# Optimization experiments

Hardware: AMD Instinct MI355X
Metric: run time of the kernel (lower is better)

## Reference

```python
import jax, jax.numpy as jnp
import numpy as np

N_NODES = 50000
N_EDGES = 800000
D = 128


def _gcn_layer(x, src, dst, deg_inv_sqrt, W, b, n_nodes):
    # GCNConv: X' = D^{-1/2} (A + I) D^{-1/2} X W + b   (PyG default, self-loops added)
    h = x @ W  # [N, D]
    norm = deg_inv_sqrt[src] * deg_inv_sqrt[dst]  # [E+N]
    msgs = h[src] * norm[:, None]  # [E+N, D] gather + scale
    out = jax.ops.segment_sum(msgs, dst, num_segments=n_nodes)  # scatter-add
    return out + b


def setup_inputs() -> dict:
    key = jax.random.key(0)
    k1, k2, k3, k4 = jax.random.split(key, 4)
    x = jax.random.normal(k1, (N_NODES, D), dtype=jnp.float32)
    edge_index = jax.random.randint(k2, (2, N_EDGES), 0, N_NODES, dtype=jnp.int64)
    scale = 1.0 / np.sqrt(D)
    W1 = jax.random.normal(k3, (D, D), dtype=jnp.float32) * scale
    b1 = jnp.zeros((D,), dtype=jnp.float32)
    W2 = jax.random.normal(k4, (D, D), dtype=jnp.float32) * scale
    b2 = jnp.zeros((D,), dtype=jnp.float32)
    return {"x": x, "edge_index": edge_index, "W1": W1, "b1": b1, "W2": W2, "b2": b2}


def reference(x, edge_index, W1, b1, W2, b2):
    n_nodes = x.shape[0]
    # add self-loops once (same graph both layers)
    loop = jnp.arange(n_nodes, dtype=edge_index.dtype)
    src = jnp.concatenate([edge_index[0], loop])
    dst = jnp.concatenate([edge_index[1], loop])
    deg = jax.ops.segment_sum(jnp.ones_like(dst, dtype=x.dtype), dst, num_segments=n_nodes)
    deg_inv_sqrt = jnp.where(deg > 0, jax.lax.rsqrt(deg), 0.0)

    h = _gcn_layer(x, src, dst, deg_inv_sqrt, W1, b1, n_nodes)
    h = jax.nn.relu(h)
    h = _gcn_layer(h, src, dst, deg_inv_sqrt, W2, b2, n_nodes)
    h = jax.nn.relu(h)
    return h
```

## Files before the change

### kernel.cpp

```cpp
#include <hip/hip_runtime.h>

#define N_NODES 50000
#define N_EDGES 800000
#define D 128
#define NB 392
#define CHUNK 2048
#define NBKT 391
#define LHM (NBKT * NB)
#define NSB ((LHM + 255) / 256)

typedef unsigned int uint32;
typedef unsigned short ushort;
typedef __attribute__((ext_vector_type(8))) short s8v;
typedef __attribute__((ext_vector_type(4))) float f4v;

__device__ __forceinline__ ushort f2bf(float f) {
    unsigned u = __float_as_uint(f);
    u += 0x7FFFu + ((u >> 16) & 1u);
    return (ushort)(u >> 16);
}
__device__ __forceinline__ float bf_lo(uint32 u) { return __uint_as_float(u << 16); }
__device__ __forceinline__ float bf_hi(uint32 u) { return __uint_as_float(u & 0xFFFF0000u); }

__device__ __forceinline__ int block_incl_scan(int v, int t) {
    int lane = t & 63, wv = t >> 6;
    int incl = v;
    #pragma unroll
    for (int off = 1; off < 64; off <<= 1) {
        int u = __shfl_up(incl, off, 64);
        if (lane >= off) incl += u;
    }
    __shared__ int wsums[4];
    if (lane == 63) wsums[wv] = incl;
    __syncthreads();
    int add = 0;
    if (wv > 0) add += wsums[0];
    if (wv > 1) add += wsums[1];
    if (wv > 2) add += wsums[2];
    return incl + add;
}

__global__ __launch_bounds__(256) void phaseA_kernel(const int* __restrict__ dst,
                                                     int* __restrict__ histM,
                                                     const float* __restrict__ W1,
                                                     const float* __restrict__ W2,
                                                     ushort* __restrict__ W1t,
                                                     ushort* __restrict__ W2t) {
    __shared__ int cnt[NBKT];
    int t = threadIdx.x, blk = blockIdx.x;
    if (blk >= NB) {
        const float* W = (blk - NB) ? W2 : W1;
        ushort* Wt = (blk - NB) ? W2t : W1t;
        #pragma unroll
        for (int it = 0; it < 16; it++) {
            int fid = t + it * 256;
            int k = fid >> 5;
            int n0 = (fid & 31) * 4;
            float4 w = ((const float4*)W)[fid];
            Wt[(n0 + 0) * D + k] = f2bf(w.x);
            Wt[(n0 + 1) * D + k] = f2bf(w.y);
            Wt[(n0 + 2) * D + k] = f2bf(w.z);
            Wt[(n0 + 3) * D + k] = f2bf(w.w);
        }
        return;
    }
    for (int i = t; i < NBKT; i += 256) cnt[i] = 0;
    __syncthreads();
    int e0 = blk * CHUNK;
    for (int i = t; i < CHUNK; i += 256) {
        int e = e0 + i;
        if (e < N_EDGES) atomicAdd(&cnt[dst[e] >> 7], 1);
    }
    __syncthreads();
    for (int i = t; i < NBKT; i += 256)
        histM[i * NB + blk] = cnt[i];
}

__global__ __launch_bounds__(256) void scan1g(const int* __restrict__ in,
                                              int* __restrict__ out,
                                              int* __restrict__ bsum) {
    int t = threadIdx.x, blk = blockIdx.x;
    int i = blk * 256 + t;
    int v = (i < LHM) ? in[i] : 0;
    int incl = block_incl_scan(v, t);
    if (i < LHM) out[i] = incl - v;
    if (t == 255) bsum[blk] = incl;
}

__global__ __launch_bounds__(256) void scan23g(int* __restrict__ out,
                                               const int* __restrict__ bsum) {
    int t = threadIdx.x, blk = blockIdx.x;
    int local = 0;
    for (int i = t; i < blk; i += 256) local += bsum[i];
    int lane = t & 63, wv = t >> 6;
    #pragma unroll
    for (int off = 32; off > 0; off >>= 1) local += __shfl_down(local, off, 64);
    __shared__ int ws[4];
    if (lane == 0) ws[wv] = local;
    __syncthreads();
    int boff = ws[0] + ws[1] + ws[2] + ws[3];
    int i = blk * 256 + t;
    if (i < LHM) out[i] += boff;
}

__global__ __launch_bounds__(256) void phaseC_kernel(const int* __restrict__ src,
                                                     const int* __restrict__ dst,
                                                     const int* __restrict__ base,
                                                     uint32* __restrict__ edgeTmp) {
    __shared__ int cur[NBKT];
    int t = threadIdx.x, blk = blockIdx.x;
    for (int i = t; i < NBKT; i += 256) cur[i] = base[i * NB + blk];
    __syncthreads();
    int e0 = blk * CHUNK;
    for (int i = t; i < CHUNK; i += 256) {
        int e = e0 + i;
        if (e < N_EDGES) {
            uint32 s = (uint32)src[e], d = (uint32)dst[e];
            int p = atomicAdd(&cur[d >> 7], 1);
            edgeTmp[p] = (s << 16) | d;
        }
    }
}

__global__ __launch_bounds__(256) void phaseD_kernel(const uint32* __restrict__ edgeTmp,
                                                     const int* __restrict__ base,
                                                     int* __restrict__ rowstart,
                                                     float* __restrict__ dis,
                                                     ushort* __restrict__ e16) {
    __shared__ int cnt[128];
    __shared__ int cur[128];
    int t = threadIdx.x, b = blockIdx.x;
    int beg = base[b * NB];
    int end = (b == NBKT - 1) ? N_EDGES : base[(b + 1) * NB];
    if (t < 128) cnt[t] = 0;
    __syncthreads();
    for (int p = beg + t; p < end; p += 256)
        atomicAdd(&cnt[edgeTmp[p] & 127], 1);
    __syncthreads();
    int c = (t < 128) ? cnt[t] : 0;
    int incl = block_incl_scan(c, t);
    int excl = incl - c;
    int node = b * 128 + t;
    if (t <= 128 && node <= N_NODES) {
        if (t < 128) rowstart[node] = beg + excl;
    }
    if (t == 128 && node <= N_NODES) rowstart[node] = end;
    if (t < 128 && node < N_NODES) dis[node] = rsqrtf((float)(c + 1));
    if (t < 128) cur[t] = excl;
    __syncthreads();
    for (int p = beg + t; p < end; p += 256) {
        uint32 u = edgeTmp[p];
        int r = atomicAdd(&cur[u & 127], 1);
        e16[beg + r] = (ushort)(u >> 16);
    }
}

template<bool BF16IN>
__global__ __launch_bounds__(256) void gemm_mfma(const void* __restrict__ Xv,
                                                 const ushort* __restrict__ Wt,
                                                 const float* __restrict__ dis,
                                                 ushort* __restrict__ Hb) {
    __shared__ ushort Cs[128 * 136];
    int t = threadIdx.x;
    int wv = t >> 6, lane = t & 63;
    int q = lane >> 4, m = lane & 15;
    int rbase = blockIdx.x * 128 + wv * 32;
    f4v zero = {0.f, 0.f, 0.f, 0.f};
    f4v acc[2][8];
    #pragma unroll
    for (int mt = 0; mt < 2; mt++)
        #pragma unroll
        for (int n = 0; n < 8; n++) acc[mt][n] = zero;

    #pragma unroll
    for (int kt = 0; kt < 4; kt++) {
        int k0 = kt * 32 + q * 8;
        s8v a[2];
        #pragma unroll
        for (int mt = 0; mt < 2; mt++) {
            int row = rbase + mt * 16 + m;
            if (row >= N_NODES) row = N_NODES - 1;
            if (BF16IN) {
                const ushort* xp = (const ushort*)Xv + (size_t)row * D + k0;
                a[mt] = *(const s8v*)xp;
            } else {
                const float* xp = (const float*)Xv + (size_t)row * D + k0;
                float4 u0 = *(const float4*)xp;
                float4 u1 = *(const float4*)(xp + 4);
                s8v av;
                av[0] = (short)f2bf(u0.x); av[1] = (short)f2bf(u0.y);
                av[2] = (short)f2bf(u0.z); av[3] = (short)f2bf(u0.w);
                av[4] = (short)f2bf(u1.x); av[5] = (short)f2bf(u1.y);
                av[6] = (short)f2bf(u1.z); av[7] = (short)f2bf(u1.w);
                a[mt] = av;
            }
        }
        #pragma unroll
        for (int n = 0; n < 8; n++) {
            s8v b = *(const s8v*)(Wt + (size_t)(n * 16 + m) * D + k0);
            acc[0][n] = __builtin_amdgcn_mfma_f32_16x16x32_bf16(a[0], b, acc[0][n], 0, 0, 0);
            acc[1][n] = __builtin_amdgcn_mfma_f32_16x16x32_bf16(a[1], b, acc[1][n], 0, 0, 0);
        }
    }
    float disv[2][4];
    #pragma unroll
    for (int mt = 0; mt < 2; mt++)
        #pragma unroll
        for (int r = 0; r < 4; r++) {
            int row = rbase + mt * 16 + q * 4 + r;
            if (row >= N_NODES) row = N_NODES - 1;
            disv[mt][r] = dis[row];
        }
    #pragma unroll
    for (int mt = 0; mt < 2; mt++)
        #pragma unroll
        for (int n = 0; n < 8; n++)
            #pragma unroll
            for (int r = 0; r < 4; r++) {
                int row = wv * 32 + mt * 16 + q * 4 + r;
                Cs[row * 136 + n * 16 + m] = f2bf(acc[mt][n][r] * disv[mt][r]);
            }
    __syncthreads();
    int gbase = blockIdx.x * 128;
    #pragma unroll
    for (int it = 0; it < 8; it++) {
        int cid = t + it * 256;
        int row = cid >> 4, off = (cid & 15) * 8;
        int grow = gbase + row;
        if (grow < N_NODES) {
            s8v v = *(const s8v*)(Cs + row * 136 + off);
            *(s8v*)(Hb + (size_t)grow * D + off) = v;
        }
    }
}

__device__ __forceinline__ void acc8(float* a, uint4 v) {
    a[0] += bf_lo(v.x); a[1] += bf_hi(v.x);
    a[2] += bf_lo(v.y); a[3] += bf_hi(v.y);
    a[4] += bf_lo(v.z); a[5] += bf_hi(v.z);
    a[6] += bf_lo(v.w); a[7] += bf_hi(v.w);
}

template<bool BF16OUT>
__global__ __launch_bounds__(256) void aggr_kernel(const uint4* __restrict__ Hb4,
                                                   const float* __restrict__ dis,
                                                   const int* __restrict__ rowstart,
                                                   const ushort* __restrict__ e16,
                                                   const float* __restrict__ bias,
                                                   void* __restrict__ Hout) {
    int t = threadIdx.x;
    int li = t & 15;
    int n = blockIdx.x * 16 + (t >> 4);
    float dn = dis[n];
    float a[8];
    {
        uint4 sv = Hb4[(size_t)n * 16 + li];
        a[0] = bf_lo(sv.x); a[1] = bf_hi(sv.x);
        a[2] = bf_lo(sv.y); a[3] = bf_hi(sv.y);
        a[4] = bf_lo(sv.z); a[5] = bf_hi(sv.z);
        a[6] = bf_lo(sv.w); a[7] = bf_hi(sv.w);
    }
    int beg = rowstart[n], end = rowstart[n + 1];
    int p = beg;
    for (; p + 7 < end; p += 8) {
        int s[8];
        #pragma unroll
        for (int j = 0; j < 8; j++) s[j] = e16[p + j];
        uint4 v[8];
        #pragma unroll
        for (int j = 0; j < 8; j++) v[j] = Hb4[(size_t)s[j] * 16 + li];
        #pragma unroll
        for (int j = 0; j < 8; j++) acc8(a, v[j]);
    }
    for (; p + 3 < end; p += 4) {
        int s0 = e16[p + 0], s1 = e16[p + 1], s2 = e16[p + 2], s3 = e16[p + 3];
        uint4 v0 = Hb4[(size_t)s0 * 16 + li];
        uint4 v1 = Hb4[(size_t)s1 * 16 + li];
        uint4 v2 = Hb4[(size_t)s2 * 16 + li];
        uint4 v3 = Hb4[(size_t)s3 * 16 + li];
        acc8(a, v0); acc8(a, v1); acc8(a, v2); acc8(a, v3);
    }
    for (; p < end; p++) {
        uint4 v0 = Hb4[(size_t)e16[p] * 16 + li];
        acc8(a, v0);
    }
    const float4* b4 = (const float4*)bias;
    float4 bb0 = b4[li * 2], bb1 = b4[li * 2 + 1];
    float r0 = fmaxf(fmaf(dn, a[0], bb0.x), 0.f);
    float r1 = fmaxf(fmaf(dn, a[1], bb0.y), 0.f);
    float r2 = fmaxf(fmaf(dn, a[2], bb0.z), 0.f);
    float r3 = fmaxf(fmaf(dn, a[3], bb0.w), 0.f);
    float r4 = fmaxf(fmaf(dn, a[4], bb1.x), 0.f);
    float r5 = fmaxf(fmaf(dn, a[5], bb1.y), 0.f);
    float r6 = fmaxf(fmaf(dn, a[6], bb1.z), 0.f);
    float r7 = fmaxf(fmaf(dn, a[7], bb1.w), 0.f);
    if (BF16OUT) {
        uint4 o;
        o.x = (uint32)f2bf(r0) | ((uint32)f2bf(r1) << 16);
        o.y = (uint32)f2bf(r2) | ((uint32)f2bf(r3) << 16);
        o.z = (uint32)f2bf(r4) | ((uint32)f2bf(r5) << 16);
        o.w = (uint32)f2bf(r6) | ((uint32)f2bf(r7) << 16);
        ((uint4*)Hout)[(size_t)n * 16 + li] = o;
    } else {
        float4* H4 = (float4*)Hout;
        float4 o0; o0.x = r0; o0.y = r1; o0.z = r2; o0.w = r3;
        float4 o1; o1.x = r4; o1.y = r5; o1.z = r6; o1.w = r7;
        H4[(size_t)n * 32 + li * 2]     = o0;
        H4[(size_t)n * 32 + li * 2 + 1] = o1;
    }
}

extern "C" void kernel_launch(void* const* d_in, const int* in_sizes, int n_in,
                              void* d_out, int out_size, void* d_ws, size_t ws_size,
                              hipStream_t stream) {
    const float* x  = (const float*)d_in[0];
    const int*   ei = (const int*)d_in[1];
    const float* W1 = (const float*)d_in[2];
    const float* b1 = (const float*)d_in[3];
    const float* W2 = (const float*)d_in[4];
    const float* b2 = (const float*)d_in[5];
    float* out = (float*)d_out;

    char* ws = (char*)d_ws;
    size_t off = 0;
    auto alloc = [&](size_t bytes) -> void* {
        void* p = ws + off;
        off += (bytes + 255) & ~(size_t)255;
        return p;
    };
    int*    histM    = (int*)alloc((size_t)LHM * 4);
    int*    base     = (int*)alloc((size_t)LHM * 4);
    int*    bsum     = (int*)alloc((size_t)NSB * 4);
    int*    rowstart = (int*)alloc((size_t)(N_NODES + 1) * 4);
    float*  dis      = (float*)alloc((size_t)N_NODES * 4);
    uint32* edgeTmp  = (uint32*)alloc((size_t)N_EDGES * 4);
    ushort* e16      = (ushort*)alloc((size_t)N_EDGES * 2);
    ushort* Hb       = (ushort*)alloc((size_t)N_NODES * D * 2);
    ushort* HO1      = (ushort*)alloc((size_t)N_NODES * D * 2);
    ushort* W1t      = (ushort*)alloc((size_t)D * D * 2);
    ushort* W2t      = (ushort*)alloc((size_t)D * D * 2);

    const int* src = ei;
    const int* dst = ei + N_EDGES;

    phaseA_kernel<<<NB + 2, 256, 0, stream>>>(dst, histM, W1, W2, W1t, W2t);
    scan1g<<<NSB, 256, 0, stream>>>(histM, base, bsum);
    scan23g<<<NSB, 256, 0, stream>>>(base, bsum);
    phaseC_kernel<<<NB, 256, 0, stream>>>(src, dst, base, edgeTmp);
    phaseD_kernel<<<NBKT, 256, 0, stream>>>(edgeTmp, base, rowstart, dis, e16);

    gemm_mfma<false><<<(N_NODES + 127) / 128, 256, 0, stream>>>(x, W1t, dis, Hb);
    aggr_kernel<true><<<N_NODES / 16, 256, 0, stream>>>((const uint4*)Hb, dis, rowstart,
                                                        e16, b1, HO1);
    gemm_mfma<true><<<(N_NODES + 127) / 128, 256, 0, stream>>>(HO1, W2t, dis, Hb);
    aggr_kernel<false><<<N_NODES / 16, 256, 0, stream>>>((const uint4*)Hb, dis, rowstart,
                                                         e16, b2, out);
}
```

Baseline: 209.5 us.

## Replace per-block histogram scan with global bucket counters and overlap GEMM1 with edge scatter

The bucket counting switches from a per-block histogram matrix with a two-kernel scan to global atomic counters plus a single-block scan, and the scatter grabs offsets with global atomics. The first GEMM now runs in the same launch as the edge scatter, which removes launches and lets the two overlap. The source-side degree normalization moves from the GEMM epilogue into the aggregation loop as a per-edge dis weight, which is what lets GEMM1 run before the degrees exist. The cost is an extra gathered dis load per edge, and the edge order within a bucket is no longer deterministic.

```diff
diff --git a/kernel.cpp b/kernel.cpp
--- a/kernel.cpp
+++ b/kernel.cpp
@@ -6,8 +6,7 @@
 #define NB 392
 #define CHUNK 2048
 #define NBKT 391
-#define LHM (NBKT * NB)
-#define NSB ((LHM + 255) / 256)
+#define GB ((N_NODES + 127) / 128)
 
 typedef unsigned int uint32;
 typedef unsigned short ushort;
@@ -40,13 +39,12 @@
     return incl + add;
 }
 
-__global__ __launch_bounds__(256) void phaseA_kernel(const int* __restrict__ dst,
-                                                     int* __restrict__ histM,
-                                                     const float* __restrict__ W1,
-                                                     const float* __restrict__ W2,
-                                                     ushort* __restrict__ W1t,
-                                                     ushort* __restrict__ W2t) {
-    __shared__ int cnt[NBKT];
+__global__ __launch_bounds__(256) void prep_kernel(const int* __restrict__ dst,
+                                                   int* __restrict__ cnt,
+                                                   const float* __restrict__ W1,
+                                                   const float* __restrict__ W2,
+                                                   ushort* __restrict__ W1t,
+                                                   ushort* __restrict__ W2t) {
     int t = threadIdx.x, blk = blockIdx.x;
     if (blk >= NB) {
         const float* W = (blk - NB) ? W2 : W1;
@@ -64,107 +62,46 @@
         }
         return;
     }
-    for (int i = t; i < NBKT; i += 256) cnt[i] = 0;
+    __shared__ int lc[NBKT];
+    for (int i = t; i < NBKT; i += 256) lc[i] = 0;
     __syncthreads();
     int e0 = blk * CHUNK;
-    for (int i = t; i < CHUNK; i += 256) {
-        int e = e0 + i;
-        if (e < N_EDGES) atomicAdd(&cnt[dst[e] >> 7], 1);
-    }
-    __syncthreads();
-    for (int i = t; i < NBKT; i += 256)
-        histM[i * NB + blk] = cnt[i];
-}
-
-__global__ __launch_bounds__(256) void scan1g(const int* __restrict__ in,
-                                              int* __restrict__ out,
-                                              int* __restrict__ bsum) {
-    int t = threadIdx.x, blk = blockIdx.x;
-    int i = blk * 256 + t;
-    int v = (i < LHM) ? in[i] : 0;
-    int incl = block_incl_scan(v, t);
-    if (i < LHM) out[i] = incl - v;
-    if (t == 255) bsum[blk] = incl;
-}
-
-__global__ __launch_bounds__(256) void scan23g(int* __restrict__ out,
-                                               const int* __restrict__ bsum) {
-    int t = threadIdx.x, blk = blockIdx.x;
-    int local = 0;
-    for (int i = t; i < blk; i += 256) local += bsum[i];
-    int lane = t & 63, wv = t >> 6;
-    #pragma unroll
-    for (int off = 32; off > 0; off >>= 1) local += __shfl_down(local, off, 64);
-    __shared__ int ws[4];
-    if (lane == 0) ws[wv] = local;
-    __syncthreads();
-    int boff = ws[0] + ws[1] + ws[2] + ws[3];
-    int i = blk * 256 + t;
-    if (i < LHM) out[i] += boff;
-}
-
-__global__ __launch_bounds__(256) void phaseC_kernel(const int* __restrict__ src,
-                                                     const int* __restrict__ dst,
-                                                     const int* __restrict__ base,
-                                                     uint32* __restrict__ edgeTmp) {
-    __shared__ int cur[NBKT];
-    int t = threadIdx.x, blk = blockIdx.x;
-    for (int i = t; i < NBKT; i += 256) cur[i] = base[i * NB + blk];
-    __syncthreads();
-    int e0 = blk * CHUNK;
-    for (int i = t; i < CHUNK; i += 256) {
-        int e = e0 + i;
-        if (e < N_EDGES) {
-            uint32 s = (uint32)src[e], d = (uint32)dst[e];
-            int p = atomicAdd(&cur[d >> 7], 1);
-            edgeTmp[p] = (s << 16) | d;
-        }
-    }
-}
-
-__global__ __launch_bounds__(256) void phaseD_kernel(const uint32* __restrict__ edgeTmp,
-                                                     const int* __restrict__ base,
-                                                     int* __restrict__ rowstart,
-                                                     float* __restrict__ dis,
-                                                     ushort* __restrict__ e16) {
-    __shared__ int cnt[128];
-    __shared__ int cur[128];
-    int t = threadIdx.x, b = blockIdx.x;
-    int beg = base[b * NB];
-    int end = (b == NBKT - 1) ? N_EDGES : base[(b + 1) * NB];
-    if (t < 128) cnt[t] = 0;
-    __syncthreads();
-    for (int p = beg + t; p < end; p += 256)
-        atomicAdd(&cnt[edgeTmp[p] & 127], 1);
-    __syncthreads();
-    int c = (t < 128) ? cnt[t] : 0;
-    int incl = block_incl_scan(c, t);
-    int excl = incl - c;
-    int node = b * 128 + t;
-    if (t <= 128 && node <= N_NODES) {
-        if (t < 128) rowstart[node] = beg + excl;
-    }
-    if (t == 128 && node <= N_NODES) rowstart[node] = end;
-    if (t < 128 && node < N_NODES) dis[node] = rsqrtf((float)(c + 1));
-    if (t < 128) cur[t] = excl;
-    __syncthreads();
-    for (int p = beg + t; p < end; p += 256) {
-        uint32 u = edgeTmp[p];
-        int r = atomicAdd(&cur[u & 127], 1);
-        e16[beg + r] = (ushort)(u >> 16);
-    }
+    #pragma unroll
+    for (int j = 0; j < 8; j++) {
+        int e = e0 + t + j * 256;
+        if (e < N_EDGES) atomicAdd(&lc[dst[e] >> 7], 1);
+    }
+    __syncthreads();
+    for (int i = t; i < NBKT; i += 256) {
+        int c = lc[i];
+        if (c) atomicAdd(&cnt[i], c);
+    }
+}
+
+__global__ __launch_bounds__(256) void scanB_kernel(const int* __restrict__ cnt,
+                                                    int* __restrict__ base,
+                                                    int* __restrict__ gcur) {
+    int t = threadIdx.x;
+    int i0 = 2 * t, i1 = 2 * t + 1;
+    int c0 = (i0 < NBKT) ? cnt[i0] : 0;
+    int c1 = (i1 < NBKT) ? cnt[i1] : 0;
+    int s = c0 + c1;
+    int incl = block_incl_scan(s, t);
+    int excl = incl - s;
+    if (i0 < NBKT) { base[i0] = excl;      gcur[i0] = excl; }
+    if (i1 < NBKT) { base[i1] = excl + c0; gcur[i1] = excl + c0; }
+    if (t == 255) base[NBKT] = incl;
 }
 
 template<bool BF16IN>
-__global__ __launch_bounds__(256) void gemm_mfma(const void* __restrict__ Xv,
-                                                 const ushort* __restrict__ Wt,
-                                                 const float* __restrict__ dis,
-                                                 ushort* __restrict__ Hb) {
+__device__ __forceinline__ void gemm_body(const void* __restrict__ Xv,
+                                          const ushort* __restrict__ Wt,
+                                          ushort* __restrict__ Hb, int bt) {
     __shared__ ushort Cs[128 * 136];
     int t = threadIdx.x;
     int wv = t >> 6, lane = t & 63;
     int q = lane >> 4, m = lane & 15;
-    int rbase = blockIdx.x * 128 + wv * 32;
+    int rbase = bt * 128 + wv * 32;
     f4v zero = {0.f, 0.f, 0.f, 0.f};
     f4v acc[2][8];
     #pragma unroll
@@ -202,15 +139,6 @@
             acc[1][n] = __builtin_amdgcn_mfma_f32_16x16x32_bf16(a[1], b, acc[1][n], 0, 0, 0);
         }
     }
-    float disv[2][4];
-    #pragma unroll
-    for (int mt = 0; mt < 2; mt++)
-        #pragma unroll
-        for (int r = 0; r < 4; r++) {
-            int row = rbase + mt * 16 + q * 4 + r;
-            if (row >= N_NODES) row = N_NODES - 1;
-            disv[mt][r] = dis[row];
-        }
     #pragma unroll
     for (int mt = 0; mt < 2; mt++)
         #pragma unroll
@@ -218,10 +146,10 @@
             #pragma unroll
             for (int r = 0; r < 4; r++) {
                 int row = wv * 32 + mt * 16 + q * 4 + r;
-                Cs[row * 136 + n * 16 + m] = f2bf(acc[mt][n][r] * disv[mt][r]);
+                Cs[row * 136 + n * 16 + m] = f2bf(acc[mt][n][r]);
             }
     __syncthreads();
-    int gbase = blockIdx.x * 128;
+    int gbase = bt * 128;
     #pragma unroll
     for (int it = 0; it < 8; it++) {
         int cid = t + it * 256;
@@ -234,11 +162,86 @@
     }
 }
 
-__device__ __forceinline__ void acc8(float* a, uint4 v) {
-    a[0] += bf_lo(v.x); a[1] += bf_hi(v.x);
-    a[2] += bf_lo(v.y); a[3] += bf_hi(v.y);
-    a[4] += bf_lo(v.z); a[5] += bf_hi(v.z);
-    a[6] += bf_lo(v.w); a[7] += bf_hi(v.w);
+__global__ __launch_bounds__(256) void phaseC_gemm1(const int* __restrict__ src,
+                                                    const int* __restrict__ dst,
+                                                    int* __restrict__ gcur,
+                                                    uint32* __restrict__ edgeTmp,
+                                                    const float* __restrict__ X,
+                                                    const ushort* __restrict__ W1t,
+                                                    ushort* __restrict__ Hb) {
+    if (blockIdx.x >= NB) {
+        gemm_body<false>(X, W1t, Hb, blockIdx.x - NB);
+        return;
+    }
+    __shared__ int lcnt[NBKT];
+    __shared__ int lcur[NBKT];
+    int t = threadIdx.x, blk = blockIdx.x;
+    for (int i = t; i < NBKT; i += 256) lcnt[i] = 0;
+    __syncthreads();
+    int e0 = blk * CHUNK;
+    uint32 rec[8]; int bk[8];
+    #pragma unroll
+    for (int j = 0; j < 8; j++) {
+        int e = e0 + t + j * 256;
+        if (e < N_EDGES) {
+            uint32 s = (uint32)src[e], d = (uint32)dst[e];
+            rec[j] = (s << 16) | d;
+            bk[j] = (int)(d >> 7);
+            atomicAdd(&lcnt[bk[j]], 1);
+        } else bk[j] = -1;
+    }
+    __syncthreads();
+    for (int i = t; i < NBKT; i += 256) {
+        int c = lcnt[i];
+        lcur[i] = c ? atomicAdd(&gcur[i], c) : 0;
+    }
+    __syncthreads();
+    #pragma unroll
+    for (int j = 0; j < 8; j++) {
+        if (bk[j] >= 0) {
+            int p = atomicAdd(&lcur[bk[j]], 1);
+            edgeTmp[p] = rec[j];
+        }
+    }
+}
+
+__global__ __launch_bounds__(256) void phaseD_kernel(const uint32* __restrict__ edgeTmp,
+                                                     const int* __restrict__ base,
+                                                     int* __restrict__ rowstart,
+                                                     float* __restrict__ dis,
+                                                     ushort* __restrict__ e16) {
+    __shared__ int cnt[128];
+    __shared__ int cur[128];
+    int t = threadIdx.x, b = blockIdx.x;
+    int beg = base[b];
+    int end = base[b + 1];
+    if (t < 128) cnt[t] = 0;
+    __syncthreads();
+    for (int p = beg + t; p < end; p += 256)
+        atomicAdd(&cnt[edgeTmp[p] & 127], 1);
+    __syncthreads();
+    int c = (t < 128) ? cnt[t] : 0;
+    int incl = block_incl_scan(c, t);
+    int excl = incl - c;
+    int node = b * 128 + t;
+    if (t < 128) {
+        if (node <= N_NODES) rowstart[node] = beg + excl;
+        if (node < N_NODES) dis[node] = rsqrtf((float)(c + 1));
+        cur[t] = excl;
+    }
+    __syncthreads();
+    for (int p = beg + t; p < end; p += 256) {
+        uint32 u = edgeTmp[p];
+        int r = atomicAdd(&cur[u & 127], 1);
+        e16[beg + r] = (ushort)(u >> 16);
+    }
+}
+
+__device__ __forceinline__ void fma8(float* a, uint4 v, float w) {
+    a[0] = fmaf(bf_lo(v.x), w, a[0]); a[1] = fmaf(bf_hi(v.x), w, a[1]);
+    a[2] = fmaf(bf_lo(v.y), w, a[2]); a[3] = fmaf(bf_hi(v.y), w, a[3]);
+    a[4] = fmaf(bf_lo(v.z), w, a[4]); a[5] = fmaf(bf_hi(v.z), w, a[5]);
+    a[6] = fmaf(bf_lo(v.w), w, a[6]); a[7] = fmaf(bf_hi(v.w), w, a[7]);
 }
 
 template<bool BF16OUT>
@@ -252,13 +255,10 @@
     int li = t & 15;
     int n = blockIdx.x * 16 + (t >> 4);
     float dn = dis[n];
-    float a[8];
+    float a[8] = {0.f, 0.f, 0.f, 0.f, 0.f, 0.f, 0.f, 0.f};
     {
         uint4 sv = Hb4[(size_t)n * 16 + li];
-        a[0] = bf_lo(sv.x); a[1] = bf_hi(sv.x);
-        a[2] = bf_lo(sv.y); a[3] = bf_hi(sv.y);
-        a[4] = bf_lo(sv.z); a[5] = bf_hi(sv.z);
-        a[6] = bf_lo(sv.w); a[7] = bf_hi(sv.w);
+        fma8(a, sv, dn);
     }
     int beg = rowstart[n], end = rowstart[n + 1];
     int p = beg;
@@ -266,23 +266,19 @@
         int s[8];
         #pragma unroll
         for (int j = 0; j < 8; j++) s[j] = e16[p + j];
+        float w[8];
+        #pragma unroll
+        for (int j = 0; j < 8; j++) w[j] = dis[s[j]];
         uint4 v[8];
         #pragma unroll
         for (int j = 0; j < 8; j++) v[j] = Hb4[(size_t)s[j] * 16 + li];
         #pragma unroll
-        for (int j = 0; j < 8; j++) acc8(a, v[j]);
-    }
-    for (; p + 3 < end; p += 4) {
-        int s0 = e16[p + 0], s1 = e16[p + 1], s2 = e16[p + 2], s3 = e16[p + 3];
+        for (int j = 0; j < 8; j++) fma8(a, v[j], w[j]);
+    }
+    for (; p < end; p++) {
+        int s0 = e16[p];
         uint4 v0 = Hb4[(size_t)s0 * 16 + li];
-        uint4 v1 = Hb4[(size_t)s1 * 16 + li];
-        uint4 v2 = Hb4[(size_t)s2 * 16 + li];
-        uint4 v3 = Hb4[(size_t)s3 * 16 + li];
-        acc8(a, v0); acc8(a, v1); acc8(a, v2); acc8(a, v3);
-    }
-    for (; p < end; p++) {
-        uint4 v0 = Hb4[(size_t)e16[p] * 16 + li];
-        acc8(a, v0);
+        fma8(a, v0, dis[s0]);
     }
     const float4* b4 = (const float4*)bias;
     float4 bb0 = b4[li * 2], bb1 = b4[li * 2 + 1];
@@ -310,6 +306,12 @@
     }
 }
 
+__global__ __launch_bounds__(256) void gemm2_kernel(const ushort* __restrict__ X,
+                                                    const ushort* __restrict__ W2t,
+                                                    ushort* __restrict__ Hb) {
+    gemm_body<true>(X, W2t, Hb, blockIdx.x);
+}
+
 extern "C" void kernel_launch(void* const* d_in, const int* in_sizes, int n_in,
                               void* d_out, int out_size, void* d_ws, size_t ws_size,
                               hipStream_t stream) {
@@ -328,9 +330,9 @@
         off += (bytes + 255) & ~(size_t)255;
         return p;
     };
-    int*    histM    = (int*)alloc((size_t)LHM * 4);
-    int*    base     = (int*)alloc((size_t)LHM * 4);
-    int*    bsum     = (int*)alloc((size_t)NSB * 4);
+    int*    cnt      = (int*)alloc((size_t)NBKT * 4);
+    int*    base     = (int*)alloc((size_t)(NBKT + 1) * 4);
+    int*    gcur     = (int*)alloc((size_t)NBKT * 4);
     int*    rowstart = (int*)alloc((size_t)(N_NODES + 1) * 4);
     float*  dis      = (float*)alloc((size_t)N_NODES * 4);
     uint32* edgeTmp  = (uint32*)alloc((size_t)N_EDGES * 4);
@@ -343,16 +345,16 @@
     const int* src = ei;
     const int* dst = ei + N_EDGES;
 
-    phaseA_kernel<<<NB + 2, 256, 0, stream>>>(dst, histM, W1, W2, W1t, W2t);
-    scan1g<<<NSB, 256, 0, stream>>>(histM, base, bsum);
-    scan23g<<<NSB, 256, 0, stream>>>(base, bsum);
-    phaseC_kernel<<<NB, 256, 0, stream>>>(src, dst, base, edgeTmp);
+    hipMemsetAsync(cnt, 0, (size_t)NBKT * 4, stream);
+
+    prep_kernel<<<NB + 2, 256, 0, stream>>>(dst, cnt, W1, W2, W1t, W2t);
+    scanB_kernel<<<1, 256, 0, stream>>>(cnt, base, gcur);
+    phaseC_gemm1<<<NB + GB, 256, 0, stream>>>(src, dst, gcur, edgeTmp, x, W1t, Hb);
     phaseD_kernel<<<NBKT, 256, 0, stream>>>(edgeTmp, base, rowstart, dis, e16);
 
-    gemm_mfma<false><<<(N_NODES + 127) / 128, 256, 0, stream>>>(x, W1t, dis, Hb);
     aggr_kernel<true><<<N_NODES / 16, 256, 0, stream>>>((const uint4*)Hb, dis, rowstart,
                                                         e16, b1, HO1);
-    gemm_mfma<true><<<(N_NODES + 127) / 128, 256, 0, stream>>>(HO1, W2t, dis, Hb);
+    gemm2_kernel<<<GB, 256, 0, stream>>>(HO1, W2t, Hb);
     aggr_kernel<false><<<N_NODES / 16, 256, 0, stream>>>((const uint4*)Hb, dis, rowstart,
                                                          e16, b2, out);
 }
```

Result: slower. 227.5 us (+8.6%).
